# Optimization experiments

Measured on AMD Instinct MI355X. Metric: run time of the kernel, lower is better.

Reference implementation:

```python
import jax, jax.numpy as jnp
import numpy as np

N_NODES = 100000
N_EDGES = 1600000
C = 128          # in_channels
H = 32           # hidden MLP width
D = 1            # Dirichlet concentration dims
T = 3            # Taylor params (estimate_bpr=True)
JITTER = 1e-20


def gcn_conv(x, W, b, edge_index, n_nodes):
    """PyG GCNConv: add self-loops, symmetric normalization, aggregate to target."""
    h = x @ W                                   # [N, C] transform first (smaller than gathering raw x then transforming per-edge)
    src = jnp.concatenate([edge_index[0], jnp.arange(n_nodes)])
    dst = jnp.concatenate([edge_index[1], jnp.arange(n_nodes)])
    deg = jax.ops.segment_sum(jnp.ones_like(dst, dtype=h.dtype), dst, num_segments=n_nodes)
    dinv = jnp.where(deg > 0, jax.lax.rsqrt(deg), 0.0)
    norm = dinv[src] * dinv[dst]                # [E+N]
    msg = h[src] * norm[:, None]                # gather + scale  [E+N, C]
    out = jax.ops.segment_sum(msg, dst, num_segments=n_nodes)  # scatter-add
    return out + b


def setup_inputs() -> dict:
    key = jax.random.key(0)
    ks = jax.random.split(key, 20)
    s = 1.0 / np.sqrt(C)
    sh = 1.0 / np.sqrt(H)
    x = jax.random.normal(ks[0], (N_NODES, C), dtype=jnp.float32)
    edge_index = jax.random.randint(ks[1], (2, N_EDGES), 0, N_NODES)
    p = {
        "x": x, "edge_index": edge_index,
        # actor params
        "a_conv_W": jax.random.uniform(ks[2], (C, C), jnp.float32, -s, s),
        "a_conv_b": jnp.zeros((C,), jnp.float32),
        "a_l1_W": jax.random.uniform(ks[3], (C, H), jnp.float32, -s, s),
        "a_l1_b": jax.random.uniform(ks[4], (H,), jnp.float32, -s, s),
        "a_l2_W": jax.random.uniform(ks[5], (H, H), jnp.float32, -sh, sh),
        "a_l2_b": jax.random.uniform(ks[6], (H,), jnp.float32, -sh, sh),
        "a_l3_W": jax.random.uniform(ks[7], (H, D + T), jnp.float32, -sh, sh),
        "a_l3_b": jax.random.uniform(ks[8], (D + T,), jnp.float32, -sh, sh),
        # critic params
        "c_conv_W": jax.random.uniform(ks[9], (C, C), jnp.float32, -s, s),
        "c_conv_b": jnp.zeros((C,), jnp.float32),
        "c_l1_W": jax.random.uniform(ks[10], (C, H), jnp.float32, -s, s),
        "c_l1_b": jax.random.uniform(ks[11], (H,), jnp.float32, -s, s),
        "c_l2_W": jax.random.uniform(ks[12], (H, H), jnp.float32, -sh, sh),
        "c_l2_b": jax.random.uniform(ks[13], (H,), jnp.float32, -sh, sh),
        "c_l3_W": jax.random.uniform(ks[14], (H, 1), jnp.float32, -sh, sh),
        "c_l3_b": jax.random.uniform(ks[15], (1,), jnp.float32, -sh, sh),
    }
    return p


def reference(x, edge_index,
              a_conv_W, a_conv_b, a_l1_W, a_l1_b, a_l2_W, a_l2_b, a_l3_W, a_l3_b,
              c_conv_W, c_conv_b, c_l1_W, c_l1_b, c_l2_W, c_l2_b, c_l3_W, c_l3_b):
    n = x.shape[0]
    # ---- actor (GNNActor.forward) ----
    a = jax.nn.relu(gcn_conv(x, a_conv_W, a_conv_b, edge_index, n)) + x   # residual
    a = jax.nn.relu(a @ a_l1_W + a_l1_b)
    a = jax.nn.relu(a @ a_l2_W + a_l2_b)
    a_out = a @ a_l3_W + a_l3_b                      # [N, D+T]
    concentration = jax.nn.softplus(a_out[:, :D]).reshape(-1) + JITTER
    taylor_params = jax.nn.softplus(a_out[:, D:]) + JITTER
    # ---- critic (GNNCritic.forward) ----
    c = jax.nn.relu(gcn_conv(x, c_conv_W, c_conv_b, edge_index, n)) + x
    c = jnp.sum(c, axis=0)                           # graph readout [C]
    c = jax.nn.relu(c @ c_l1_W + c_l1_b)
    c = jax.nn.relu(c @ c_l2_W + c_l2_b)
    value = c @ c_l3_W + c_l3_b                      # [1]
    return concentration, taylor_params, value
```

## Files before the change

### kernel.cpp

```cpp
#include <hip/hip_runtime.h>
#include <math.h>

#define CCH 128
#define HID 32
#define SLOTS 64
#define NBINS 782
#define BSHIFT 7
#define BCAP 2432

typedef __attribute__((ext_vector_type(8))) short bf16x8;
typedef __attribute__((ext_vector_type(4))) float f32x4;

__device__ __forceinline__ unsigned bf16pk(float a, float b) {
    unsigned ua = __builtin_bit_cast(unsigned, a);
    unsigned ub = __builtin_bit_cast(unsigned, b);
    ua = (ua + 0x7FFFu + ((ua >> 16) & 1u)) >> 16;
    ub = (ub + 0x7FFFu + ((ub >> 16) & 1u)) >> 16;
    return ua | (ub << 16);
}
__device__ __forceinline__ unsigned short bf16s(float a) {
    unsigned ua = __builtin_bit_cast(unsigned, a);
    ua = (ua + 0x7FFFu + ((ua >> 16) & 1u)) >> 16;
    return (unsigned short)ua;
}
__device__ __forceinline__ float bflo(unsigned v) {
    return __builtin_bit_cast(float, v << 16);
}
__device__ __forceinline__ float bfhiF(unsigned v) {
    return __builtin_bit_cast(float, v & 0xFFFF0000u);
}

__global__ void k_zero(const float* __restrict__ aW, const float* __restrict__ cW,
                       unsigned short* __restrict__ Wt,
                       float* __restrict__ csum, int* __restrict__ binCnt,
                       unsigned short* __restrict__ xsb, int N) {
    int t = threadIdx.x;
    if (blockIdx.x == 0) {
        if (t < CCH) csum[t] = 0.f;
        for (int i = t; i < NBINS; i += 256) binCnt[i] = 0;
        if (t < 64) ((unsigned*)xsb)[(long)N * 64 + t] = 0u;
        return;
    }
    int id = (blockIdx.x - 1) * 256 + t;
    int conv = id >> 14;
    int rem = id & 16383;
    int n = rem >> 7;
    int k = rem & 127;
    const float* W = conv ? cW : aW;
    Wt[id] = bf16s(W[k * CCH + n]);
}

__global__ __launch_bounds__(256, 4)
void k_bin(const int* __restrict__ ei, int E,
           int* __restrict__ binCnt, unsigned* __restrict__ stage) {
    int t = threadIdx.x;
    __shared__ int lcnt[NBINS];
    __shared__ int lofs[NBINS];
    const int nchunk = (E + 2047) / 2048;
    for (int ch = blockIdx.x; ch < nchunk; ch += gridDim.x) {
        int base = ch * 2048;
        for (int i = t; i < NBINS; i += 256) lcnt[i] = 0;
        __syncthreads();
        unsigned pk[8]; int bin[8];
#pragma unroll
        for (int k = 0; k < 8; k++) {
            int e = base + k * 256 + t;
            if (e < E) {
                unsigned src = (unsigned)ei[e];
                unsigned dst = (unsigned)ei[E + e];
                bin[k] = dst >> BSHIFT;
                pk[k] = src | ((dst & 0x7Fu) << 17);
                atomicAdd(&lcnt[bin[k]], 1);
            } else bin[k] = -1;
        }
        __syncthreads();
        for (int i = t; i < NBINS; i += 256) {
            int c = lcnt[i];
            lofs[i] = c ? atomicAdd(&binCnt[i], c) : 0;
        }
        __syncthreads();
#pragma unroll
        for (int k = 0; k < 8; k++) {
            if (bin[k] >= 0) {
                int pos = atomicAdd(&lofs[bin[k]], 1);
                if (pos < BCAP)
                    stage[(long)bin[k] * BCAP + pos] = pk[k];
            }
        }
        __syncthreads();
    }
}

__global__ __launch_bounds__(256)
void k_place(const unsigned* __restrict__ stage, const int* __restrict__ binCnt,
             const float* __restrict__ x, int* __restrict__ cnt,
             int* __restrict__ csr, unsigned short* __restrict__ xsb,
             float* __restrict__ csum, int N) {
    __shared__ int lcnt[128];
    __shared__ int lofs[128];
    __shared__ int lcur[128];
    __shared__ int wtot[2];
    __shared__ float scs[CCH];
    __shared__ unsigned ssrc[BCAP];
    __shared__ unsigned short sd8[BCAP];

    int t = threadIdx.x;
    int b = blockIdx.x;
    int count = binCnt[b];
    if (count > BCAP) count = BCAP;
    const unsigned* sp = stage + (long)b * BCAP;
    int dbase = b << BSHIFT;

    if (t < 128) lcnt[t] = 0;
    __syncthreads();
    for (int i = t; i < count; i += 256)
        atomicAdd(&lcnt[sp[i] >> 17], 1);
    __syncthreads();

    int craw = (t < 128) ? lcnt[t] : 0;
    int cc = craw > SLOTS ? SLOTS : craw;
    int lane = t & 63, wv = t >> 6;
    int xsc = cc;
#pragma unroll
    for (int d = 1; d < 64; d <<= 1) {
        int y = __shfl_up(xsc, d, 64);
        if (lane >= d) xsc += y;
    }
    if (t < 128 && lane == 63) wtot[wv] = xsc;
    __syncthreads();
    if (t < 128) {
        int pre = wv ? wtot[0] : 0;
        int excl = pre + xsc - cc;
        lofs[t] = excl;
        lcur[t] = excl;
        cnt[dbase + t] = craw;
    }
    __syncthreads();
    int total = wtot[0] + wtot[1];

    for (int i = t; i < count; i += 256) {
        unsigned p = sp[i];
        int d8 = (int)(p >> 17);
        int pos = atomicAdd(&lcur[d8], 1);
        if (pos - lofs[d8] < SLOTS) {
            ssrc[pos] = (p & 0x1FFFFu) << 5;
            sd8[pos] = (unsigned short)d8;
        }
    }
    __syncthreads();

    for (int i = t; i < total; i += 256) {
        int d8 = sd8[i];
        csr[(long)(dbase + d8) * SLOTS + (i - lofs[d8])] = (int)ssrc[i];
    }

    int rows = N - dbase; if (rows > 128) rows = 128;
    int nf4 = rows * 32;
    const float4* x4 = (const float4*)(x + (long)dbase * CCH);
    uint2* xo = (uint2*)xsb + (long)dbase * 32;
    float c0 = 0.f, c1 = 0.f, c2 = 0.f, c3 = 0.f;
    for (int i = t; i < nf4; i += 256) {
        float dv = rsqrtf((float)lcnt[i >> 5] + 1.0f);
        float4 v = x4[i];
        c0 += v.x; c1 += v.y; c2 += v.z; c3 += v.w;
        uint2 p;
        p.x = bf16pk(dv * v.x, dv * v.y);
        p.y = bf16pk(dv * v.z, dv * v.w);
        xo[i] = p;
    }
    if (t < CCH) scs[t] = 0.f;
    __syncthreads();
    int c4 = (t & 31) * 4;
    atomicAdd(&scs[c4 + 0], c0);
    atomicAdd(&scs[c4 + 1], c1);
    atomicAdd(&scs[c4 + 2], c2);
    atomicAdd(&scs[c4 + 3], c3);
    __syncthreads();
    if (t < CCH) atomicAdd(&csum[t], scs[t]);
}

__global__ __launch_bounds__(256, 4)
void k_gather_y(const unsigned short* __restrict__ xs,
                const int* __restrict__ cnt,
                const int* __restrict__ csr,
                unsigned short* __restrict__ yb, int N) {
    int t = threadIdx.x;
    int lane = t & 63;
    int wid = t >> 6;
    int half = lane >> 5;
    int hl = lane & 31;
    int wg = blockIdx.x * 4 + wid;
    int stride = gridDim.x * 4;
    const uint2* xu = (const uint2*)xs;
    uint2* yu = (uint2*)yb;
    int npairs = N >> 1;
    int zoff = N << 5;

    for (int p = wg; p < npairs; p += stride) {
        int nA = p * 2;
        int degr = cnt[nA + half];
        float dvd = rsqrtf((float)degr + 1.0f);
        int deg = degr > SLOTS ? SLOTS : degr;
        int degA = __builtin_amdgcn_readlane(deg, 0);
        int degB = __builtin_amdgcn_readlane(deg, 32);
        int dmax = degA > degB ? degA : degB;
        dmax = __builtin_amdgcn_readfirstlane(dmax);

        int idxl = csr[(long)nA * SLOTS + lane + (lane & 32)];
        if (hl >= deg) idxl = zoff;

        uint2 vs = xu[(long)nA * 32 + lane];
        float a0 = bflo(vs.x), a1 = bfhiF(vs.x);
        float a2 = bflo(vs.y), a3 = bfhiF(vs.y);

        int dm = dmax < 32 ? dmax : 32;
        int dm8 = (dm + 7) & ~7;
        for (int e = 0; e < dm8; e += 8) {
            uint2 v[8];
#pragma unroll
            for (int k = 0; k < 8; k++) {
                int iA = __builtin_amdgcn_readlane(idxl, e + k);
                int iB = __builtin_amdgcn_readlane(idxl, 32 + e + k);
                int boff = half ? iB : iA;
                v[k] = xu[boff + hl];
            }
#pragma unroll
            for (int k = 0; k < 8; k++) {
                a0 += bflo(v[k].x);
                a1 += __builtin_bit_cast(float, v[k].x);
                a2 += bflo(v[k].y);
                a3 += __builtin_bit_cast(float, v[k].y);
            }
        }
        if (dmax > 32) {
            int idxh = csr[(long)nA * SLOTS + lane + (lane & 32) + 32];
            if (hl + 32 >= deg) idxh = zoff;
            int dx8 = (dmax + 7) & ~7;
            for (int e = 32; e < dx8; e += 8) {
                uint2 w[8];
#pragma unroll
                for (int k = 0; k < 8; k++) {
                    int iA = __builtin_amdgcn_readlane(idxh, e - 32 + k);
                    int iB = __builtin_amdgcn_readlane(idxh, e + k);
                    int boff = half ? iB : iA;
                    w[k] = xu[boff + hl];
                }
#pragma unroll
                for (int k = 0; k < 8; k++) {
                    a0 += bflo(w[k].x);
                    a1 += __builtin_bit_cast(float, w[k].x);
                    a2 += bflo(w[k].y);
                    a3 += __builtin_bit_cast(float, w[k].y);
                }
            }
        }
        uint2 o;
        o.x = bf16pk(dvd * a0, dvd * a1);
        o.y = bf16pk(dvd * a2, dvd * a3);
        yu[(long)nA * 32 + lane] = o;
    }
}

__global__ __launch_bounds__(256, 4)
void k_gemm_y(const unsigned short* __restrict__ yb,
              const unsigned short* __restrict__ xs,
              const int* __restrict__ cnt,
              const unsigned short* __restrict__ Wt,
              const float* __restrict__ ab, const float* __restrict__ cb,
              unsigned short* __restrict__ a1b, float* __restrict__ csum,
              int N, int gblocks) {
    __shared__ unsigned short Ws[128 * 128];
    __shared__ float scs[CCH];
    int t = threadIdx.x;
    int bid = blockIdx.x;
    int conv = bid >= gblocks ? 1 : 0;
    int row0 = (conv ? bid - gblocks : bid) * 128;
    int wid = t >> 6, lane = t & 63;
    int m = lane & 15, quad = lane >> 4;
    int mrow0 = row0 + wid * 32;

    bf16x8 afr[2][4];
#pragma unroll
    for (int rt = 0; rt < 2; rt++) {
        int row = mrow0 + rt * 16 + m; if (row >= N) row = N - 1;
        const unsigned short* yr = yb + (long)row * CCH;
#pragma unroll
        for (int ks = 0; ks < 4; ks++)
            afr[rt][ks] = *(const bf16x8*)(yr + ks * 32 + quad * 8);
    }

    {
        const uint4* src = (const uint4*)(Wt + conv * 16384);
#pragma unroll
        for (int i = 0; i < 8; i++) {
            int id = i * 256 + t;
            int n = id >> 4, c = id & 15;
            uint4 v = src[id];
            *(uint4*)(Ws + n * 128 + ((c ^ (n & 15)) * 8)) = v;
        }
        if (conv && t < CCH) scs[t] = 0.f;
    }
    __syncthreads();

    if (conv == 0) {
#pragma unroll
        for (int nt = 0; nt < 8; nt++) {
            int n = nt * 16 + m;
            f32x4 ac0 = {0.f, 0.f, 0.f, 0.f};
            f32x4 ac1 = {0.f, 0.f, 0.f, 0.f};
#pragma unroll
            for (int ks = 0; ks < 4; ks++) {
                bf16x8 b = *(const bf16x8*)(Ws + n * 128 + (((ks * 4 + quad) ^ m) * 8));
                ac0 = __builtin_amdgcn_mfma_f32_16x16x32_bf16(afr[0][ks], b, ac0, 0, 0, 0);
                ac1 = __builtin_amdgcn_mfma_f32_16x16x32_bf16(afr[1][ks], b, ac1, 0, 0, 0);
            }
            float bias = ab[n];
            __syncthreads();
            unsigned short* reg = Ws + nt * 2048;
#pragma unroll
            for (int h = 0; h < 2; h++) {
#pragma unroll
                for (int r = 0; r < 4; r++) {
                    int rl = wid * 32 + quad * 4 + r + h * 16;
                    float acv = h ? ac1[r] : ac0[r];
                    reg[rl * 16 + m] = bf16s(fmaxf(acv + bias, 0.f));
                }
            }
        }
        __syncthreads();
#pragma unroll
        for (int it = 0; it < 8; it++) {
            int g = it * 256 + t;
            int rl = g >> 4;
            int c8 = g & 15;
            int row = row0 + rl;
            if (row < N) {
                const unsigned short* lp = Ws + (c8 >> 1) * 2048 + rl * 16 + (c8 & 1) * 8;
                uint4 lv = *(const uint4*)lp;
                float rd = sqrtf((float)cnt[row] + 1.0f);
                uint4 xv = *(const uint4*)(xs + (long)row * CCH + c8 * 8);
                unsigned lw[4] = {lv.x, lv.y, lv.z, lv.w};
                unsigned xw[4] = {xv.x, xv.y, xv.z, xv.w};
                uint4 o;
                unsigned ow[4];
#pragma unroll
                for (int q = 0; q < 4; q++) {
                    float r0 = bflo(lw[q]) + rd * bflo(xw[q]);
                    float r1 = bfhiF(lw[q]) + rd * bfhiF(xw[q]);
                    ow[q] = bf16pk(r0, r1);
                }
                o.x = ow[0]; o.y = ow[1]; o.z = ow[2]; o.w = ow[3];
                *(uint4*)(a1b + (long)row * CCH + c8 * 8) = o;
            }
        }
    } else {
#pragma unroll
        for (int nt = 0; nt < 8; nt++) {
            int n = nt * 16 + m;
            f32x4 ac0 = {0.f, 0.f, 0.f, 0.f};
            f32x4 ac1 = {0.f, 0.f, 0.f, 0.f};
#pragma unroll
            for (int ks = 0; ks < 4; ks++) {
                bf16x8 b = *(const bf16x8*)(Ws + n * 128 + (((ks * 4 + quad) ^ m) * 8));
                ac0 = __builtin_amdgcn_mfma_f32_16x16x32_bf16(afr[0][ks], b, ac0, 0, 0, 0);
                ac1 = __builtin_amdgcn_mfma_f32_16x16x32_bf16(afr[1][ks], b, ac1, 0, 0, 0);
            }
            float bias = cb[n];
            float part = 0.f;
#pragma unroll
            for (int h = 0; h < 2; h++) {
#pragma unroll
                for (int r = 0; r < 4; r++) {
                    int row = mrow0 + quad * 4 + r + h * 16;
                    float acv = h ? ac1[r] : ac0[r];
                    if (row < N) part += fmaxf(acv + bias, 0.f);
                }
            }
            atomicAdd(&scs[n], part);
        }
        __syncthreads();
        if (t < CCH) atomicAdd(&csum[t], scs[t]);
    }
}

__device__ __forceinline__ float softplus_f(float v) {
    return fmaxf(v, 0.f) + log1pf(expf(-fabsf(v)));
}

__global__ __launch_bounds__(256, 3)
void k_mlp(const unsigned short* __restrict__ a1b,
           const float* __restrict__ W1, const float* __restrict__ b1,
           const float* __restrict__ W2, const float* __restrict__ b2,
           const float* __restrict__ W3, const float* __restrict__ b3,
           const float* __restrict__ csum,
           const float* __restrict__ cW1, const float* __restrict__ cb1,
           const float* __restrict__ cW2, const float* __restrict__ cb2,
           const float* __restrict__ cW3, const float* __restrict__ cb3,
           float* __restrict__ out, int N) {
    __shared__ unsigned rowsW[64 * 65];
    __shared__ float h1L[64 * 33];
    __shared__ float h2L[64 * 33];
    int t = threadIdx.x;
    int l = t & 63;
    int w = t >> 6;
    long nbase = (long)blockIdx.x * 64;

    const uint4* ga = (const uint4*)(a1b + nbase * CCH);
#pragma unroll
    for (int i = 0; i < 4; i++) {
        int idx = i * 256 + t;
        int node = idx >> 4;
        int ch = idx & 15;
        uint4 v = make_uint4(0, 0, 0, 0);
        if (nbase + node < N) v = ga[node * 16 + ch];
        unsigned* dst = &rowsW[node * 65 + ch * 4];
        dst[0] = v.x; dst[1] = v.y; dst[2] = v.z; dst[3] = v.w;
    }
    __syncthreads();

    int j0 = __builtin_amdgcn_readfirstlane(w * 8);

    float h1[8];
#pragma unroll
    for (int j = 0; j < 8; j++) h1[j] = b1[j0 + j];
    for (int kp = 0; kp < 64; kp++) {
        unsigned v = rowsW[l * 65 + kp];
        float f0 = __builtin_bit_cast(float, v << 16);
        float f1 = __builtin_bit_cast(float, v & 0xFFFF0000u);
        const float* w0 = W1 + (2 * kp) * HID + j0;
        const float* w1 = W1 + (2 * kp + 1) * HID + j0;
#pragma unroll
        for (int j = 0; j < 8; j++)
            h1[j] = fmaf(f1, w1[j], fmaf(f0, w0[j], h1[j]));
    }
#pragma unroll
    for (int j = 0; j < 8; j++) h1L[l * 33 + j0 + j] = fmaxf(h1[j], 0.f);
    __syncthreads();

    float h2[8];
#pragma unroll
    for (int j = 0; j < 8; j++) h2[j] = b2[j0 + j];
    for (int k = 0; k < HID; k++) {
        float hv = h1L[l * 33 + k];
        const float* wr = W2 + k * HID + j0;
#pragma unroll
        for (int j = 0; j < 8; j++)
            h2[j] = fmaf(hv, wr[j], h2[j]);
    }
#pragma unroll
    for (int j = 0; j < 8; j++) h2L[l * 33 + j0 + j] = fmaxf(h2[j], 0.f);
    __syncthreads();

    if (w == 0) {
        long node = nbase + l;
        if (node < N) {
            float o[4] = {b3[0], b3[1], b3[2], b3[3]};
            for (int k = 0; k < HID; k++) {
                float hv = h2L[l * 33 + k];
#pragma unroll
                for (int m = 0; m < 4; m++)
                    o[m] = fmaf(hv, W3[k * 4 + m], o[m]);
            }
            out[node] = softplus_f(o[0]) + 1e-20f;
            float* ty = out + N;
            ty[node * 3 + 0] = softplus_f(o[1]) + 1e-20f;
            ty[node * 3 + 1] = softplus_f(o[2]) + 1e-20f;
            ty[node * 3 + 2] = softplus_f(o[3]) + 1e-20f;
        }
    }

    if (blockIdx.x == 0) {
        __syncthreads();
        float* cv  = h1L;
        float* hh1 = h2L;
        float* hh2 = h2L + 64;
        if (t < CCH) cv[t] = csum[t];
        __syncthreads();
        if (t < HID) {
            float a = cb1[t];
            for (int k = 0; k < CCH; k++) a = fmaf(cv[k], cW1[k * HID + t], a);
            hh1[t] = fmaxf(a, 0.f);
        }
        __syncthreads();
        if (t < HID) {
            float a = cb2[t];
            for (int k = 0; k < HID; k++) a = fmaf(hh1[k], cW2[k * HID + t], a);
            hh2[t] = fmaxf(a, 0.f);
        }
        __syncthreads();
        if (t == 0) {
            float a = cb3[0];
            for (int k = 0; k < HID; k++) a = fmaf(hh2[k], cW3[k], a);
            out[(long)4 * N] = a;
        }
    }
}

extern "C" void kernel_launch(void* const* d_in, const int* in_sizes, int n_in,
                              void* d_out, int out_size, void* d_ws, size_t ws_size,
                              hipStream_t stream) {
    const float* x   = (const float*)d_in[0];
    const int*   ei  = (const int*)d_in[1];
    const float* aW  = (const float*)d_in[2];
    const float* ab  = (const float*)d_in[3];
    const float* aW1 = (const float*)d_in[4];
    const float* ab1 = (const float*)d_in[5];
    const float* aW2 = (const float*)d_in[6];
    const float* ab2 = (const float*)d_in[7];
    const float* aW3 = (const float*)d_in[8];
    const float* ab3 = (const float*)d_in[9];
    const float* cW  = (const float*)d_in[10];
    const float* cb  = (const float*)d_in[11];
    const float* cW1 = (const float*)d_in[12];
    const float* cb1 = (const float*)d_in[13];
    const float* cW2 = (const float*)d_in[14];
    const float* cb2 = (const float*)d_in[15];
    const float* cW3 = (const float*)d_in[16];
    const float* cb3 = (const float*)d_in[17];
    float* out = (float*)d_out;

    const int N = in_sizes[0] / CCH;
    const int E = in_sizes[1] / 2;

    char* ws = (char*)d_ws;
    size_t off = 0;
    auto take = [&](size_t bytes) { void* p = ws + off; off += (bytes + 255) & ~(size_t)255; return p; };
    int*            cnt    = (int*)           take((size_t)NBINS * 128 * 4);
    int*            binCnt = (int*)           take(NBINS * 4);
    float*          csum   = (float*)         take(CCH * 4);
    unsigned short* Wt     = (unsigned short*)take(2 * 16384 * 2);
    int*            csr    = (int*)           take((size_t)N * SLOTS * 4);
    unsigned*       stage  = (unsigned*)      take((size_t)NBINS * BCAP * 4);
    unsigned short* xsb    = (unsigned short*)take((size_t)(N + 1) * CCH * 2);
    unsigned short* ybb    = (unsigned short*)take((size_t)N * CCH * 2);
    unsigned short* a1b    = (unsigned short*)take((size_t)N * CCH * 2);
    (void)ws_size;

    k_zero<<<129, 256, 0, stream>>>(aW, cW, Wt, csum, binCnt, xsb, N);
    k_bin<<<512, 256, 0, stream>>>(ei, E, binCnt, stage);
    k_place<<<NBINS, 256, 0, stream>>>(stage, binCnt, x, cnt, csr, xsb, csum, N);

    k_gather_y<<<2048, 256, 0, stream>>>(xsb, cnt, csr, ybb, N);

    const int gblocks = (N + 127) / 128;
    k_gemm_y<<<gblocks * 2, 256, 0, stream>>>(ybb, xsb, cnt, Wt, ab, cb, a1b,
                                              csum, N, gblocks);

    k_mlp<<<(N + 63) / 64, 256, 0, stream>>>(a1b, aW1, ab1, aW2, ab2, aW3, ab3,
                                             csum, cW1, cb1, cW2, cb2, cW3, cb3,
                                             out, N);
}
```

Baseline: 320.6 us.

## Fuse actor MLP head into GCN GEMM epilogue and split value head

The actor's post-conv residual rows are no longer written to a global bf16 buffer and read back by a separate MLP kernel. They are kept in shared memory, and the three-layer MLP plus softplus outputs are computed in the same block that ran the GEMM. The critic readout MLP moves into its own tiny single-block kernel. This removes a 25 MB write and read round trip and one large launch, but it adds shared memory per block, lowers launch bounds occupancy from 4 to 3, and makes each actor block do serial MLP work.

```diff
diff --git a/kernel.cpp b/kernel.cpp
--- a/kernel.cpp
+++ b/kernel.cpp
@@ -261,15 +261,23 @@
     }
 }
 
-__global__ __launch_bounds__(256, 4)
-void k_gemm_y(const unsigned short* __restrict__ yb,
-              const unsigned short* __restrict__ xs,
-              const int* __restrict__ cnt,
-              const unsigned short* __restrict__ Wt,
-              const float* __restrict__ ab, const float* __restrict__ cb,
-              unsigned short* __restrict__ a1b, float* __restrict__ csum,
-              int N, int gblocks) {
+__device__ __forceinline__ float softplus_f(float v) {
+    return fmaxf(v, 0.f) + log1pf(expf(-fabsf(v)));
+}
+
+__global__ __launch_bounds__(256, 3)
+void k_gemm_mlp(const unsigned short* __restrict__ yb,
+                const unsigned short* __restrict__ xs,
+                const int* __restrict__ cnt,
+                const unsigned short* __restrict__ Wt,
+                const float* __restrict__ ab, const float* __restrict__ cb,
+                const float* __restrict__ W1, const float* __restrict__ b1,
+                const float* __restrict__ W2, const float* __restrict__ b2,
+                const float* __restrict__ W3, const float* __restrict__ b3,
+                float* __restrict__ csum, float* __restrict__ out,
+                int N, int gblocks) {
     __shared__ unsigned short Ws[128 * 128];
+    __shared__ float h1L[128 * 33];
     __shared__ float scs[CCH];
     int t = threadIdx.x;
     int bid = blockIdx.x;
@@ -335,13 +343,12 @@
             int c8 = g & 15;
             int row = row0 + rl;
             if (row < N) {
-                const unsigned short* lp = Ws + (c8 >> 1) * 2048 + rl * 16 + (c8 & 1) * 8;
+                unsigned short* lp = Ws + (c8 >> 1) * 2048 + rl * 16 + (c8 & 1) * 8;
                 uint4 lv = *(const uint4*)lp;
                 float rd = sqrtf((float)cnt[row] + 1.0f);
                 uint4 xv = *(const uint4*)(xs + (long)row * CCH + c8 * 8);
                 unsigned lw[4] = {lv.x, lv.y, lv.z, lv.w};
                 unsigned xw[4] = {xv.x, xv.y, xv.z, xv.w};
-                uint4 o;
                 unsigned ow[4];
 #pragma unroll
                 for (int q = 0; q < 4; q++) {
@@ -349,8 +356,63 @@
                     float r1 = bfhiF(lw[q]) + rd * bfhiF(xw[q]);
                     ow[q] = bf16pk(r0, r1);
                 }
+                uint4 o;
                 o.x = ow[0]; o.y = ow[1]; o.z = ow[2]; o.w = ow[3];
-                *(uint4*)(a1b + (long)row * CCH + c8 * 8) = o;
+                *(uint4*)lp = o;
+            }
+        }
+        __syncthreads();
+        int nl = t >> 1;
+        int hp = t & 1;
+        int j0 = hp * 16;
+        const unsigned* wsu = (const unsigned*)Ws;
+        float h1[16];
+#pragma unroll
+        for (int j = 0; j < 16; j++) h1[j] = b1[j0 + j];
+        for (int i = 0; i < 64; i++) {
+            unsigned v = wsu[(i >> 3) * 1024 + nl * 8 + (i & 7)];
+            float f0 = bflo(v);
+            float f1 = bfhiF(v);
+            const float* w0 = W1 + (2 * i) * HID + j0;
+            const float* w1 = W1 + (2 * i + 1) * HID + j0;
+#pragma unroll
+            for (int j = 0; j < 16; j++)
+                h1[j] = fmaf(f1, w1[j], fmaf(f0, w0[j], h1[j]));
+        }
+#pragma unroll
+        for (int j = 0; j < 16; j++) h1L[nl * 33 + j0 + j] = fmaxf(h1[j], 0.f);
+        __syncthreads();
+
+        float h2[16];
+#pragma unroll
+        for (int j = 0; j < 16; j++) h2[j] = b2[j0 + j];
+        for (int k = 0; k < HID; k++) {
+            float hv = h1L[nl * 33 + k];
+            const float* wr = W2 + k * HID + j0;
+#pragma unroll
+            for (int j = 0; j < 16; j++)
+                h2[j] = fmaf(hv, wr[j], h2[j]);
+        }
+        __syncthreads();
+#pragma unroll
+        for (int j = 0; j < 16; j++) h1L[nl * 33 + j0 + j] = fmaxf(h2[j], 0.f);
+        __syncthreads();
+
+        if (hp == 0) {
+            long node = (long)row0 + nl;
+            if (node < N) {
+                float o[4] = {b3[0], b3[1], b3[2], b3[3]};
+                for (int k = 0; k < HID; k++) {
+                    float hv = h1L[nl * 33 + k];
+#pragma unroll
+                    for (int mm = 0; mm < 4; mm++)
+                        o[mm] = fmaf(hv, W3[k * 4 + mm], o[mm]);
+                }
+                out[node] = softplus_f(o[0]) + 1e-20f;
+                float* ty = out + N;
+                ty[node * 3 + 0] = softplus_f(o[1]) + 1e-20f;
+                ty[node * 3 + 1] = softplus_f(o[2]) + 1e-20f;
+                ty[node * 3 + 2] = softplus_f(o[3]) + 1e-20f;
             }
         }
     } else {
@@ -383,116 +445,33 @@
     }
 }
 
-__device__ __forceinline__ float softplus_f(float v) {
-    return fmaxf(v, 0.f) + log1pf(expf(-fabsf(v)));
-}
-
-__global__ __launch_bounds__(256, 3)
-void k_mlp(const unsigned short* __restrict__ a1b,
-           const float* __restrict__ W1, const float* __restrict__ b1,
-           const float* __restrict__ W2, const float* __restrict__ b2,
-           const float* __restrict__ W3, const float* __restrict__ b3,
-           const float* __restrict__ csum,
-           const float* __restrict__ cW1, const float* __restrict__ cb1,
-           const float* __restrict__ cW2, const float* __restrict__ cb2,
-           const float* __restrict__ cW3, const float* __restrict__ cb3,
-           float* __restrict__ out, int N) {
-    __shared__ unsigned rowsW[64 * 65];
-    __shared__ float h1L[64 * 33];
-    __shared__ float h2L[64 * 33];
+__global__ void k_vhead(const float* __restrict__ csum,
+                        const float* __restrict__ cW1, const float* __restrict__ cb1,
+                        const float* __restrict__ cW2, const float* __restrict__ cb2,
+                        const float* __restrict__ cW3, const float* __restrict__ cb3,
+                        float* __restrict__ out, int N) {
+    __shared__ float cv[CCH];
+    __shared__ float hh1[HID];
+    __shared__ float hh2[HID];
     int t = threadIdx.x;
-    int l = t & 63;
-    int w = t >> 6;
-    long nbase = (long)blockIdx.x * 64;
-
-    const uint4* ga = (const uint4*)(a1b + nbase * CCH);
-#pragma unroll
-    for (int i = 0; i < 4; i++) {
-        int idx = i * 256 + t;
-        int node = idx >> 4;
-        int ch = idx & 15;
-        uint4 v = make_uint4(0, 0, 0, 0);
-        if (nbase + node < N) v = ga[node * 16 + ch];
-        unsigned* dst = &rowsW[node * 65 + ch * 4];
-        dst[0] = v.x; dst[1] = v.y; dst[2] = v.z; dst[3] = v.w;
-    }
-    __syncthreads();
-
-    int j0 = __builtin_amdgcn_readfirstlane(w * 8);
-
-    float h1[8];
-#pragma unroll
-    for (int j = 0; j < 8; j++) h1[j] = b1[j0 + j];
-    for (int kp = 0; kp < 64; kp++) {
-        unsigned v = rowsW[l * 65 + kp];
-        float f0 = __builtin_bit_cast(float, v << 16);
-        float f1 = __builtin_bit_cast(float, v & 0xFFFF0000u);
-        const float* w0 = W1 + (2 * kp) * HID + j0;
-        const float* w1 = W1 + (2 * kp + 1) * HID + j0;
-#pragma unroll
-        for (int j = 0; j < 8; j++)
-            h1[j] = fmaf(f1, w1[j], fmaf(f0, w0[j], h1[j]));
-    }
-#pragma unroll
-    for (int j = 0; j < 8; j++) h1L[l * 33 + j0 + j] = fmaxf(h1[j], 0.f);
-    __syncthreads();
-
-    float h2[8];
-#pragma unroll
-    for (int j = 0; j < 8; j++) h2[j] = b2[j0 + j];
-    for (int k = 0; k < HID; k++) {
-        float hv = h1L[l * 33 + k];
-        const float* wr = W2 + k * HID + j0;
-#pragma unroll
-        for (int j = 0; j < 8; j++)
-            h2[j] = fmaf(hv, wr[j], h2[j]);
-    }
-#pragma unroll
-    for (int j = 0; j < 8; j++) h2L[l * 33 + j0 + j] = fmaxf(h2[j], 0.f);
-    __syncthreads();
-
-    if (w == 0) {
-        long node = nbase + l;
-        if (node < N) {
-            float o[4] = {b3[0], b3[1], b3[2], b3[3]};
-            for (int k = 0; k < HID; k++) {
-                float hv = h2L[l * 33 + k];
-#pragma unroll
-                for (int m = 0; m < 4; m++)
-                    o[m] = fmaf(hv, W3[k * 4 + m], o[m]);
-            }
-            out[node] = softplus_f(o[0]) + 1e-20f;
-            float* ty = out + N;
-            ty[node * 3 + 0] = softplus_f(o[1]) + 1e-20f;
-            ty[node * 3 + 1] = softplus_f(o[2]) + 1e-20f;
-            ty[node * 3 + 2] = softplus_f(o[3]) + 1e-20f;
-        }
-    }
-
-    if (blockIdx.x == 0) {
-        __syncthreads();
-        float* cv  = h1L;
-        float* hh1 = h2L;
-        float* hh2 = h2L + 64;
-        if (t < CCH) cv[t] = csum[t];
-        __syncthreads();
-        if (t < HID) {
-            float a = cb1[t];
-            for (int k = 0; k < CCH; k++) a = fmaf(cv[k], cW1[k * HID + t], a);
-            hh1[t] = fmaxf(a, 0.f);
-        }
-        __syncthreads();
-        if (t < HID) {
-            float a = cb2[t];
-            for (int k = 0; k < HID; k++) a = fmaf(hh1[k], cW2[k * HID + t], a);
-            hh2[t] = fmaxf(a, 0.f);
-        }
-        __syncthreads();
-        if (t == 0) {
-            float a = cb3[0];
-            for (int k = 0; k < HID; k++) a = fmaf(hh2[k], cW3[k], a);
-            out[(long)4 * N] = a;
-        }
+    if (t < CCH) cv[t] = csum[t];
+    __syncthreads();
+    if (t < HID) {
+        float a = cb1[t];
+        for (int k = 0; k < CCH; k++) a = fmaf(cv[k], cW1[k * HID + t], a);
+        hh1[t] = fmaxf(a, 0.f);
+    }
+    __syncthreads();
+    if (t < HID) {
+        float a = cb2[t];
+        for (int k = 0; k < HID; k++) a = fmaf(hh1[k], cW2[k * HID + t], a);
+        hh2[t] = fmaxf(a, 0.f);
+    }
+    __syncthreads();
+    if (t == 0) {
+        float a = cb3[0];
+        for (int k = 0; k < HID; k++) a = fmaf(hh2[k], cW3[k], a);
+        out[(long)4 * N] = a;
     }
 }
 
@@ -533,7 +512,6 @@
     unsigned*       stage  = (unsigned*)      take((size_t)NBINS * BCAP * 4);
     unsigned short* xsb    = (unsigned short*)take((size_t)(N + 1) * CCH * 2);
     unsigned short* ybb    = (unsigned short*)take((size_t)N * CCH * 2);
-    unsigned short* a1b    = (unsigned short*)take((size_t)N * CCH * 2);
     (void)ws_size;
 
     k_zero<<<129, 256, 0, stream>>>(aW, cW, Wt, csum, binCnt, xsb, N);
@@ -543,10 +521,9 @@
     k_gather_y<<<2048, 256, 0, stream>>>(xsb, cnt, csr, ybb, N);
 
     const int gblocks = (N + 127) / 128;
-    k_gemm_y<<<gblocks * 2, 256, 0, stream>>>(ybb, xsb, cnt, Wt, ab, cb, a1b,
-                                              csum, N, gblocks);
-
-    k_mlp<<<(N + 63) / 64, 256, 0, stream>>>(a1b, aW1, ab1, aW2, ab2, aW3, ab3,
-                                             csum, cW1, cb1, cW2, cb2, cW3, cb3,
-                                             out, N);
-}
+    k_gemm_mlp<<<gblocks * 2, 256, 0, stream>>>(ybb, xsb, cnt, Wt, ab, cb,
+                                                aW1, ab1, aW2, ab2, aW3, ab3,
+                                                csum, out, N, gblocks);
+
+    k_vhead<<<1, 128, 0, stream>>>(csum, cW1, cb1, cW2, cb2, cW3, cb3, out, N);
+}
```

Result: slower. 347.7 us (+8.4%).
